# Optimization experiments

Measured on AMD Instinct MI355X. Metric: run time of the kernel, lower is better.

Reference implementation:

```python
import jax, jax.numpy as jnp
import numpy as np

T, B, D = 64, 256, 2000
TN, E, H, A, V = 3000, 256, 256, 128, 128
PS, PE, S = 64, 64, 128
G1N, G1L, G2N, G2L = 1500, 4, 1500, 6


def setup_inputs():
    key = jax.random.key(0)
    ks = jax.random.split(key, 32)
    def nrm(k, shape, s=0.05):
        return jax.random.normal(k, shape, dtype=jnp.float32) * s
    inp = {}
    inp["X"] = jax.random.uniform(ks[0], (T, B, D), dtype=jnp.float32)
    inp["profiles"] = nrm(ks[1], (B, PS), 1.0)
    inp["ini_embd"] = nrm(ks[2], (TN, E), 1.0)
    inp["Wa_w"] = nrm(ks[3], (2 * E, A))
    inp["Wa_b"] = jnp.zeros((A,), jnp.float32)
    inp["Ua_w"] = nrm(ks[4], (A, 1))
    inp["gru_Wih"] = nrm(ks[5], (3 * H, E))
    inp["gru_Whh"] = nrm(ks[6], (3 * H, H))
    inp["gru_bih"] = jnp.zeros((3 * H,), jnp.float32)
    inp["gru_bhh"] = jnp.zeros((3 * H,), jnp.float32)
    inp["tranH_w"] = nrm(ks[7], (H + PE, E))
    inp["tranH_b"] = jnp.zeros((E,), jnp.float32)
    inp["out_w"] = nrm(ks[8], (H + V + PE, D))
    inp["out_b"] = jnp.zeros((D,), jnp.float32)
    inp["erase_w"] = nrm(ks[9], (E, V))
    inp["erase_b"] = jnp.zeros((V,), jnp.float32)
    inp["add_w"] = nrm(ks[10], (E, V))
    inp["add_b"] = jnp.zeros((V,), jnp.float32)
    inp["iniVam"] = nrm(ks[11], (S, V), 1.0)
    inp["emP_w"] = nrm(ks[12], (PS, PE))
    inp["emP_b"] = jnp.zeros((PE,), jnp.float32)
    inp["attnP_w"] = nrm(ks[13], (PE + V, PE))
    inp["attnP_b"] = jnp.zeros((PE,), jnp.float32)
    inp["KMIds"] = jax.random.randint(ks[14], (S,), 0, TN, dtype=jnp.int32)
    inp["leaves1"] = jax.random.randint(ks[15], (G1N, G1L), 0, TN, dtype=jnp.int32)
    inp["anc1"] = jax.random.randint(ks[16], (G1N, G1L), 0, TN, dtype=jnp.int32)
    inp["leaves2"] = jax.random.randint(ks[17], (G2N, G2L), 0, TN, dtype=jnp.int32)
    inp["anc2"] = jax.random.randint(ks[18], (G2N, G2L), 0, TN, dtype=jnp.int32)
    inp["mapInfo"] = jax.random.randint(ks[19], (D,), 0, G1N + G2N, dtype=jnp.int32)
    lens = jnp.sort(jax.random.randint(ks[20], (B,), 1, T + 1, dtype=jnp.int32))[::-1]
    inp["X_lengths"] = lens.at[0].set(T)
    return inp


def _forward(floats, ints):
    (X, profiles, ini_embd, Wa_w, Wa_b, Ua_w, gru_Wih, gru_Whh, gru_bih, gru_bhh,
     tranH_w, tranH_b, out_w, out_b, erase_w, erase_b, add_w, add_b, iniVam,
     emP_w, emP_b, attnP_w, attnP_b) = floats
    KMIds, leaves1, anc1, leaves2, anc2, mapInfo, X_lengths = ints

    # GRAM-style ontology attention over (leaf, ancestor) pairs, grouped by path length
    def group_embed(leaves, anc):
        le = ini_embd[leaves]                                     # [N,L,E]
        ae = ini_embd[anc]                                        # [N,L,E]
        hdn = jnp.tanh(jnp.concatenate([le, ae], axis=2) @ Wa_w + Wa_b)
        w = jax.nn.softmax(hdn @ Ua_w, axis=1)                    # [N,L,1]
        return jnp.sum(w * ae, axis=1)                            # [N,E]

    embedMat = jnp.concatenate([group_embed(leaves1, anc1),
                                group_embed(leaves2, anc2)], axis=0)[mapInfo]  # [D,E]
    Xe = jnp.einsum('tbd,de->tbe', X, embedMat)                   # [T,B,E]

    # packed-sequence GRU: frozen state / zero output beyond each sample's length
    mask = (jnp.arange(T)[:, None] < X_lengths[None, :])[..., None]  # [T,B,1]

    def gru_step(h, tup):
        x_t, m_t = tup
        gx = x_t @ gru_Wih.T + gru_bih
        gh = h @ gru_Whh.T + gru_bhh
        r = jax.nn.sigmoid(gx[:, :H] + gh[:, :H])
        z = jax.nn.sigmoid(gx[:, H:2 * H] + gh[:, H:2 * H])
        n = jnp.tanh(gx[:, 2 * H:] + r * gh[:, 2 * H:])
        h_new = (1.0 - z) * n + z * h
        h = jnp.where(m_t, h_new, h)
        return h, jnp.where(m_t, h, 0.0)

    h0 = jnp.zeros((B, H), jnp.float32)
    _, gru_out = jax.lax.scan(gru_step, h0, (Xe, mask))           # [T,B,H]

    prof = profiles @ emP_w + emP_b                               # [B,PE]
    prof_rep = jnp.broadcast_to(prof[None], (T, B, PE))
    tran = jnp.concatenate([gru_out, prof_rep], axis=2) @ tranH_w + tranH_b  # [T,B,E]
    KM = ini_embd[KMIds]                                          # [S,E]
    slot_w = jax.nn.softmax(jnp.einsum('tbe,se->tbs', tran, KM), axis=2)     # [T,B,S]

    # erase/add gates depend only on Xe -> precompute, then scan VM recurrence
    erase = jax.nn.sigmoid(Xe @ erase_w + erase_b)                # [T,B,V]
    add = jnp.tanh(Xe @ add_w + add_b)                            # [T,B,V]

    def mem_step(VM, tup):
        sw, er, ad = tup                                          # [B,S],[B,V],[B,V]
        read = jnp.einsum('bs,bsv->bv', sw, VM)
        VM = VM * (1.0 - sw[:, :, None] * er[:, None, :]) + sw[:, :, None] * ad[:, None, :]
        return VM, read

    VM0 = jnp.broadcast_to(iniVam[None], (B, S, V))
    _, read = jax.lax.scan(mem_step, VM0, (slot_w, erase, add))   # read: [T,B,V]

    attn = jax.nn.relu(jnp.concatenate([prof_rep, read], axis=2) @ attnP_w + attnP_b)
    prof2 = prof_rep * attn
    final = jnp.concatenate([gru_out, read, prof2], axis=2)       # [T,B,H+V+PE]
    # dropout is identity (eval / drop_rate=0)
    return jax.nn.softmax(final @ out_w + out_b, axis=2)          # [T,B,D]


def reference(X, profiles, ini_embd, Wa_w, Wa_b, Ua_w, gru_Wih, gru_Whh, gru_bih, gru_bhh, tranH_w, tranH_b, out_w, out_b, erase_w, erase_b, add_w, add_b, iniVam, emP_w, emP_b, attnP_w, attnP_b, KMIds, leaves1, anc1, leaves2, anc2, mapInfo, X_lengths):
    floats = (X, profiles, ini_embd, Wa_w, Wa_b, Ua_w, gru_Wih, gru_Whh, gru_bih, gru_bhh,
              tranH_w, tranH_b, out_w, out_b, erase_w, erase_b, add_w, add_b, iniVam,
              emP_w, emP_b, attnP_w, attnP_b)
    ints = (KMIds, leaves1, anc1, leaves2, anc2, mapInfo, X_lengths)
    return _forward(floats, ints)
```

## Files before the change

### kernel.cpp

```cpp
#include <hip/hip_runtime.h>
#include <hip/hip_bf16.h>
#include <cmath>

#define T_  64
#define B_  256
#define D_  2000
#define TN_ 3000
#define E_  256
#define H_  256
#define A_  128
#define V_  128
#define PS_ 64
#define PE_ 64
#define S_  128
#define G1N_ 1500
#define G1L_ 4
#define G2N_ 1500
#define G2L_ 6
#define M_  (T_ * B_)
#define KF_ (H_ + V_ + PE_)

typedef __attribute__((ext_vector_type(8))) short short8_t;
typedef __attribute__((ext_vector_type(4))) float floatx4;
typedef _Float16 __attribute__((ext_vector_type(2))) h2_t;
typedef _Float16 __attribute__((ext_vector_type(8))) h8_t;

static __device__ __forceinline__ float sigmoidf_(float x) {
    return 1.0f / (1.0f + __expf(-x));
}

static __device__ __forceinline__ void bsplit_(float v, __hip_bfloat16& hi, __hip_bfloat16& lo) {
    hi = __float2bfloat16(v);
    lo = __float2bfloat16(v - __bfloat162float(hi));
}

static __device__ __forceinline__ float dot2_(unsigned int w, unsigned int h, float acc) {
    union { unsigned int u; h2_t h; } cw, ch;
    cw.u = w; ch.u = h;
#if __has_builtin(__builtin_amdgcn_fdot2)
    return __builtin_amdgcn_fdot2(cw.h, ch.h, acc, false);
#else
    return acc + (float)cw.h[0] * (float)ch.h[0] + (float)cw.h[1] * (float)ch.h[1];
#endif
}

static __device__ __forceinline__ void gl_lds16(const void* g, void* l)
{
#if __has_builtin(__builtin_amdgcn_global_load_lds)
    __builtin_amdgcn_global_load_lds(
        (const __attribute__((address_space(1))) void*)g,
        (__attribute__((address_space(3))) void*)l, 16, 0, 0);
#else
    *(short8_t*)l = *(const short8_t*)g;
#endif
}

template<int DT>
static __device__ __forceinline__ floatx4 mfma16_(short8_t a, short8_t b, floatx4 c) {
    if constexpr (DT == 0) {
        return __builtin_amdgcn_mfma_f32_16x16x32_bf16(a, b, c, 0, 0, 0);
    } else {
        union { short8_t s; h8_t h; } ua, ub;
        ua.s = a; ub.s = b;
        return __builtin_amdgcn_mfma_f32_16x16x32_f16(ua.h, ub.h, c, 0, 0, 0);
    }
}

template<int EPI, bool ACCUM, int OUTMODE, int NPH, int DT>
__global__ __launch_bounds__(256)
void k_mgemm3(const __hip_bfloat16* __restrict__ Ahi, const __hip_bfloat16* __restrict__ Alo,
              const __hip_bfloat16* __restrict__ Bhi, const __hip_bfloat16* __restrict__ Blo,
              const float* __restrict__ bias, float* __restrict__ Cf,
              __hip_bfloat16* __restrict__ Chi, __hip_bfloat16* __restrict__ Clo,
              int K, int Nreal, int nblk)
{
    __shared__ __align__(16) short As[2][4096];
    __shared__ __align__(16) short Bs[2][4096];

    const int tid  = threadIdx.x;
    const int lane = tid & 63;
    const int w    = tid >> 6;
    const int wm   = w >> 1, wn = w & 1;
    const int lr   = lane & 15;
    const int lkc  = lane >> 4;

    const int bx = blockIdx.x;
    const int xcd = bx & 7, loc = bx >> 3;
    const int mchunk = (int)gridDim.x / (8 * nblk);
    const int m0 = (xcd * mchunk + loc / nblk) * 128;
    const int n0 = (loc % nblk) * 128;

    const int fa = 2 * w;
    const size_t aoff0 = (size_t)(m0 + fa * 16 + lr) * K + lkc * 8;
    const size_t aoff1 = aoff0 + (size_t)16 * K;
    const size_t boff0 = (size_t)(n0 + fa * 16 + lr) * K + lkc * 8;
    const size_t boff1 = boff0 + (size_t)16 * K;

    const int lA0 = (fa    ) * 512 + lane * 8;
    const int lA1 = (fa + 1) * 512 + lane * 8;

    floatx4 acc[4][4];
#pragma unroll
    for (int i = 0; i < 4; ++i)
#pragma unroll
        for (int j = 0; j < 4; ++j) acc[i][j] = floatx4{0.f, 0.f, 0.f, 0.f};

    const int KT = K >> 5;
    const int NT = NPH * KT;

    int s_ph = 0, s_k = 0;
    auto do_stage = [&](int buf) {
        const __hip_bfloat16* Ap = (s_ph == 2) ? Alo : Ahi;
        const __hip_bfloat16* Bp = (s_ph == 1) ? Blo : Bhi;
        gl_lds16(Ap + aoff0 + s_k, &As[buf][lA0]);
        gl_lds16(Ap + aoff1 + s_k, &As[buf][lA1]);
        gl_lds16(Bp + boff0 + s_k, &Bs[buf][lA0]);
        gl_lds16(Bp + boff1 + s_k, &Bs[buf][lA1]);
        s_k += 32;
        if (s_k >= K) { s_k = 0; ++s_ph; }
    };

    do_stage(0);
    __syncthreads();

#pragma unroll 1
    for (int t = 0; t < NT; ++t) {
        const int cur = t & 1;
        if (t + 1 < NT) do_stage(cur ^ 1);

        short8_t af[4], bf[4];
#pragma unroll
        for (int i = 0; i < 4; ++i)
            af[i] = *(const short8_t*)(const void*)&As[cur][(wm * 4 + i) * 512 + lane * 8];
#pragma unroll
        for (int j = 0; j < 4; ++j)
            bf[j] = *(const short8_t*)(const void*)&Bs[cur][(wn * 4 + j) * 512 + lane * 8];
#pragma unroll
        for (int i = 0; i < 4; ++i)
#pragma unroll
            for (int j = 0; j < 4; ++j)
                acc[i][j] = mfma16_<DT>(af[i], bf[j], acc[i][j]);

        __syncthreads();
    }

#pragma unroll
    for (int i = 0; i < 4; ++i) {
        const int row = m0 + wm * 64 + i * 16 + (lane >> 4) * 4;
#pragma unroll
        for (int j = 0; j < 4; ++j) {
            const int col = n0 + wn * 64 + j * 16 + (lane & 15);
            if (col < Nreal) {
                float bv = bias ? bias[col] : 0.0f;
#pragma unroll
                for (int r = 0; r < 4; ++r) {
                    float v = acc[i][j][r] + bv;
                    if (EPI == 1) v = (col < 128) ? sigmoidf_(v) : tanhf(v);
                    if (EPI == 2) {
                        if (col < 128) v = sigmoidf_(v);
                        else if (col < 256) v = tanhf(v);
                    }
                    size_t o = (size_t)(row + r) * Nreal + col;
                    if (OUTMODE == 0) {
                        if (ACCUM) v += Cf[o];
                        Cf[o] = v;
                    } else if (OUTMODE == 1) {
                        __hip_bfloat16 h, l;
                        bsplit_(v, h, l);
                        Chi[o] = h; Clo[o] = l;
                    } else {
                        ((_Float16*)Chi)[o] = (_Float16)v;
                    }
                }
            }
        }
    }
}

__global__ __launch_bounds__(256)
void k_cvtX(const float* __restrict__ X, _Float16* __restrict__ XH)
{
    int idx = blockIdx.x * blockDim.x + threadIdx.x;
    if (idx >= M_ * 256) return;
    int m = idx >> 8, d0 = (idx & 255) * 8;
    _Float16 h[8];
    if (d0 + 7 < D_) {
        float4 p = *(const float4*)(X + (size_t)m * D_ + d0);
        float4 q = *(const float4*)(X + (size_t)m * D_ + d0 + 4);
        h[0]=(_Float16)p.x; h[1]=(_Float16)p.y; h[2]=(_Float16)p.z; h[3]=(_Float16)p.w;
        h[4]=(_Float16)q.x; h[5]=(_Float16)q.y; h[6]=(_Float16)q.z; h[7]=(_Float16)q.w;
    } else {
#pragma unroll
        for (int i = 0; i < 8; ++i)
            h[i] = (d0 + i < D_) ? (_Float16)X[(size_t)m * D_ + d0 + i] : (_Float16)0.0f;
    }
    *(short8_t*)(XH + (size_t)m * 2048 + d0) = *(short8_t*)h;
}

__global__ __launch_bounds__(256)
void k_mgemmXh(const _Float16* __restrict__ XH,
               const _Float16* __restrict__ Bhi, const _Float16* __restrict__ Blo,
               __hip_bfloat16* __restrict__ Chi, __hip_bfloat16* __restrict__ Clo)
{
    const int KP = 2048, NN = 256, nblk = 2;
    __shared__ __align__(16) short Ah[2][4096];
    __shared__ __align__(16) short Bh[2][4096];
    __shared__ __align__(16) short Bl[2][4096];

    const int tid  = threadIdx.x;
    const int lane = tid & 63;
    const int w    = tid >> 6;
    const int wm   = w >> 1, wn = w & 1;
    const int lr   = lane & 15;
    const int lkc  = lane >> 4;

    const int bx = blockIdx.x;
    const int xcd = bx & 7, loc = bx >> 3;
    const int mchunk = 256 / (8 * nblk);
    const int m0 = (xcd * mchunk + loc / nblk) * 128;
    const int n0 = (loc % nblk) * 128;

    const int fa = 2 * w;
    const size_t aoff0 = (size_t)(m0 + fa * 16 + lr) * KP + lkc * 8;
    const size_t aoff1 = aoff0 + (size_t)16 * KP;
    const size_t boff0 = (size_t)(n0 + fa * 16 + lr) * KP + lkc * 8;
    const size_t boff1 = boff0 + (size_t)16 * KP;

    const int lA0 = (fa    ) * 512 + lane * 8;
    const int lA1 = (fa + 1) * 512 + lane * 8;

    floatx4 acc[4][4];
#pragma unroll
    for (int i = 0; i < 4; ++i)
#pragma unroll
        for (int j = 0; j < 4; ++j) acc[i][j] = floatx4{0.f, 0.f, 0.f, 0.f};

    int s_k = 0;
    auto do_stage = [&](int buf) {
        gl_lds16(XH  + aoff0 + s_k, &Ah[buf][lA0]);
        gl_lds16(XH  + aoff1 + s_k, &Ah[buf][lA1]);
        gl_lds16(Bhi + boff0 + s_k, &Bh[buf][lA0]);
        gl_lds16(Bhi + boff1 + s_k, &Bh[buf][lA1]);
        gl_lds16(Blo + boff0 + s_k, &Bl[buf][lA0]);
        gl_lds16(Blo + boff1 + s_k, &Bl[buf][lA1]);
        s_k += 32;
    };

    do_stage(0);
    __syncthreads();

#pragma unroll 1
    for (int t = 0; t < KP / 32; ++t) {
        const int cur = t & 1;
        if (s_k < KP) do_stage(cur ^ 1);

        short8_t af[4], bfh[4], bfl[4];
#pragma unroll
        for (int i = 0; i < 4; ++i) {
            af[i]  = *(const short8_t*)(const void*)&Ah[cur][(wm * 4 + i) * 512 + lane * 8];
            bfh[i] = *(const short8_t*)(const void*)&Bh[cur][(wn * 4 + i) * 512 + lane * 8];
        }
#pragma unroll
        for (int i = 0; i < 4; ++i)
#pragma unroll
            for (int j = 0; j < 4; ++j)
                acc[i][j] = mfma16_<1>(af[i], bfh[j], acc[i][j]);
#pragma unroll
        for (int j = 0; j < 4; ++j)
            bfl[j] = *(const short8_t*)(const void*)&Bl[cur][(wn * 4 + j) * 512 + lane * 8];
#pragma unroll
        for (int i = 0; i < 4; ++i)
#pragma unroll
            for (int j = 0; j < 4; ++j)
                acc[i][j] = mfma16_<1>(af[i], bfl[j], acc[i][j]);

        __syncthreads();
    }

#pragma unroll
    for (int i = 0; i < 4; ++i) {
        const int row = m0 + wm * 64 + i * 16 + (lane >> 4) * 4;
#pragma unroll
        for (int j = 0; j < 4; ++j) {
            const int col = n0 + wn * 64 + j * 16 + (lane & 15);
#pragma unroll
            for (int r = 0; r < 4; ++r) {
                float v = acc[i][j][r];
                size_t o = (size_t)(row + r) * NN + col;
                __hip_bfloat16 h, l;
                bsplit_(v, h, l);
                Chi[o] = h; Clo[o] = l;
            }
        }
    }
}

template<int BM, int BN, int BK, int TM, int TN>
__global__ __launch_bounds__(256)
void k_gemm(const float* __restrict__ A, const float* __restrict__ B,
            float* __restrict__ C, int M, int N, int K)
{
    __shared__ float As[BK][BM + 4];
    __shared__ float Bs[BK][BN + 4];
    const int tid = threadIdx.y * blockDim.x + threadIdx.x;
    const int m0 = blockIdx.y * BM;
    const int n0 = blockIdx.x * BN;
    float acc[TM][TN];
#pragma unroll
    for (int i = 0; i < TM; ++i)
#pragma unroll
        for (int j = 0; j < TN; ++j) acc[i][j] = 0.0f;
    for (int k0 = 0; k0 < K; k0 += BK) {
#pragma unroll
        for (int i = tid; i < BM * BK; i += 256) {
            int r = i / BK, c = i % BK;
            int m = m0 + r;
            As[c][r] = (m < M) ? A[(size_t)m * K + k0 + c] : 0.0f;
        }
#pragma unroll
        for (int i = tid; i < BK * BN; i += 256) {
            int r = i / BN, c = i % BN;
            Bs[r][c] = B[(size_t)(k0 + r) * N + n0 + c];
        }
        __syncthreads();
#pragma unroll
        for (int kk = 0; kk < BK; ++kk) {
            float a[TM], b[TN];
#pragma unroll
            for (int i = 0; i < TM; ++i) a[i] = As[kk][threadIdx.y * TM + i];
#pragma unroll
            for (int j = 0; j < TN; ++j) b[j] = Bs[kk][threadIdx.x * TN + j];
#pragma unroll
            for (int i = 0; i < TM; ++i)
#pragma unroll
                for (int j = 0; j < TN; ++j) acc[i][j] += a[i] * b[j];
        }
        __syncthreads();
    }
#pragma unroll
    for (int i = 0; i < TM; ++i) {
        int m = m0 + threadIdx.y * TM + i;
        if (m >= M) continue;
#pragma unroll
        for (int j = 0; j < TN; ++j)
            C[(size_t)m * N + n0 + threadIdx.x * TN + j] = acc[i][j];
    }
}

__global__ __launch_bounds__(256)
void k_packall(const float* __restrict__ Wa_w,
               const float* __restrict__ erase_w, const float* __restrict__ add_w,
               const float* __restrict__ Wih,
               const float* __restrict__ erase_b, const float* __restrict__ add_b,
               const float* __restrict__ bih,
               const float* __restrict__ tranH_w, const float* __restrict__ out_w,
               const float* __restrict__ ini_embd, const int* __restrict__ KMIds,
               const float* __restrict__ Whh,
               float* __restrict__ W2p,
               __hip_bfloat16* __restrict__ WGhi, __hip_bfloat16* __restrict__ WGlo,
               float* __restrict__ biasG,
               __hip_bfloat16* __restrict__ THhi, __hip_bfloat16* __restrict__ THlo,
               _Float16* __restrict__ OWf,
               __hip_bfloat16* __restrict__ KMhi, __hip_bfloat16* __restrict__ KMlo,
               unsigned int* __restrict__ W4)
{
    int idx = blockIdx.x * blockDim.x + threadIdx.x;
    if (idx < 65536) {
        int e = idx >> 8, j = idx & 255;
        W2p[idx] = (j < A_) ? Wa_w[(size_t)e * A_ + j]
                            : Wa_w[(size_t)(E_ + e) * A_ + (j - A_)];
        return;
    }
    idx -= 65536;
    if (idx < 262144) {
        int n = idx >> 8, k = idx & 255;
        float v;
        if (n < 128)      v = erase_w[(size_t)k * V_ + n];
        else if (n < 256) v = add_w[(size_t)k * V_ + (n - 128)];
        else              v = Wih[(size_t)(n - 256) * 256 + k];
        bsplit_(v, WGhi[idx], WGlo[idx]);
        return;
    }
    idx -= 262144;
    if (idx < 1024) {
        biasG[idx] = (idx < 128) ? erase_b[idx]
                   : (idx < 256) ? add_b[idx - 128]
                                 : bih[idx - 256];
        return;
    }
    idx -= 1024;
    if (idx < 81920) {
        int n = idx / 320, k = idx % 320;
        bsplit_(tranH_w[(size_t)k * 256 + n], THhi[idx], THlo[idx]);
        return;
    }
    idx -= 81920;
    if (idx < 917504) {
        int n = idx / 448, k = idx % 448;
        OWf[idx] = (n < D_) ? (_Float16)out_w[(size_t)k * D_ + n] : (_Float16)0.0f;
        return;
    }
    idx -= 917504;
    if (idx < 32768) {
        int s = idx >> 8, k = idx & 255;
        bsplit_(ini_embd[(size_t)KMIds[s] * E_ + k], KMhi[idx], KMlo[idx]);
        return;
    }
    idx -= 32768;
    if (idx < 98304) {
        int j = idx / 128, e2 = idx % 128;
        union { unsigned int u; h2_t h; } c;
        c.h[0] = (_Float16)Whh[(size_t)j * 256 + 2 * e2];
        c.h[1] = (_Float16)Whh[(size_t)j * 256 + 2 * e2 + 1];
        int ch = e2 >> 2, i = e2 & 3;
        W4[((size_t)ch * 768 + j) * 4 + i] = c.u;
    }
}

__global__ void k_prof(const float* __restrict__ profiles, const float* __restrict__ emP_w,
                       const float* __restrict__ emP_b, float* __restrict__ prof)
{
    int b = blockIdx.x, j = threadIdx.x;
    float acc = emP_b[j];
    for (int k = 0; k < PS_; ++k) acc += profiles[(size_t)b * PS_ + k] * emP_w[(size_t)k * PE_ + j];
    prof[(size_t)b * PE_ + j] = acc;
}

__global__ void k_embMT_f16(const float* __restrict__ embG, const int* __restrict__ mapInfo,
                            _Float16* __restrict__ hi, _Float16* __restrict__ lo)
{
    int idx = blockIdx.x * blockDim.x + threadIdx.x;
    if (idx >= 256 * 2048) return;
    int e = idx >> 11, d = idx & 2047;
    float v = (d < D_) ? embG[(size_t)mapInfo[d] * E_ + e] : 0.0f;
    _Float16 h = (_Float16)v;
    hi[idx] = h;
    lo[idx] = (_Float16)(v - (float)h);
}

__global__ void k_group_embed(const float* __restrict__ PP, const float* __restrict__ Wa_b,
                              const float* __restrict__ Ua_w, const float* __restrict__ ini_embd,
                              const int* __restrict__ leaves1, const int* __restrict__ anc1,
                              const int* __restrict__ leaves2, const int* __restrict__ anc2,
                              float* __restrict__ embedG)
{
    int n = blockIdx.x;
    int lane = threadIdx.x;
    const int* lv; const int* ac; int L;
    if (n < G1N_) { L = G1L_; lv = leaves1 + (size_t)n * G1L_; ac = anc1 + (size_t)n * G1L_; }
    else { int n2 = n - G1N_; L = G2L_; lv = leaves2 + (size_t)n2 * G2L_; ac = anc2 + (size_t)n2 * G2L_; }

    float score[6]; int ai[6];
    for (int l = 0; l < L; ++l) {
        int li = lv[l]; int av = ac[l]; ai[l] = av;
        float s = 0.0f;
        for (int a = lane; a < A_; a += 64) {
            float hv = tanhf(PP[(size_t)li * 256 + a] + PP[(size_t)av * 256 + 128 + a] + Wa_b[a]);
            s += hv * Ua_w[a];
        }
        for (int o = 32; o; o >>= 1) s += __shfl_xor(s, o);
        score[l] = s;
    }
    float mx = -1e30f;
    for (int l = 0; l < L; ++l) mx = fmaxf(mx, score[l]);
    float w[6], sum = 0.0f;
    for (int l = 0; l < L; ++l) { w[l] = __expf(score[l] - mx); sum += w[l]; }
    float inv = 1.0f / sum;
    for (int e = lane; e < E_; e += 64) {
        float acc = 0.0f;
        for (int l = 0; l < L; ++l) acc += w[l] * inv * ini_embd[(size_t)ai[l] * E_ + e];
        embedG[(size_t)n * E_ + e] = acc;
    }
}

__global__ __launch_bounds__(768)
void k_gru7(const float* __restrict__ Cg, const uint4* __restrict__ W4,
            const float* __restrict__ bhh, const int* __restrict__ X_len,
            const float* __restrict__ prof, _Float16* __restrict__ F,
            __hip_bfloat16* __restrict__ At_hi, __hip_bfloat16* __restrict__ At_lo)
{
    const int b = blockIdx.x;
    const int tid = threadIdx.x;

    __shared__ uint4 h2S[32];
    __shared__ float ghS[768];
    __shared__ float gxnS[256];

    if (tid < 128) ((unsigned int*)h2S)[tid] = 0u;

    float hreg = 0.0f;
    const int len = X_len[b];
    const float bj = bhh[tid];

    __hip_bfloat16 phi, plo;
    if (tid >= 256 && tid < 320)
        bsplit_(prof[(size_t)b * PE_ + (tid - 256)], phi, plo);

    __syncthreads();

#define DOT8(BUF, BASE)                                                     \
    {                                                                       \
        _Pragma("unroll")                                                   \
        for (int s = 0; s < 8; ++s) {                                       \
            uint4 h = h2S[(BASE) + s];                                      \
            a0 = dot2_(BUF[s].x, h.x, a0);                                  \
            a0 = dot2_(BUF[s].y, h.y, a0);                                  \
            a0 = dot2_(BUF[s].z, h.z, a0);                                  \
            a0 = dot2_(BUF[s].w, h.w, a0);                                  \
        }                                                                   \
    }
#define LOAD8(BUF, BASE)                                                    \
    {                                                                       \
        _Pragma("unroll")                                                   \
        for (int s = 0; s < 8; ++s)                                         \
            BUF[s] = W4[(size_t)((BASE) + s) * 768 + tid];                  \
    }

    for (int t = 0; t < T_; ++t) {
        float gxv = Cg[((size_t)t * B_ + b) * 1024 + 256 + tid];

        uint4 wa[8], wb[8];
        LOAD8(wa, 0)
        float a0 = bj;
        LOAD8(wb, 8)
        DOT8(wa, 0)
        LOAD8(wa, 16)
        DOT8(wb, 8)
        LOAD8(wb, 24)
        DOT8(wa, 16)
        DOT8(wb, 24)

        if (tid < 512) ghS[tid] = a0 + gxv;
        else { ghS[tid] = a0; gxnS[tid - 512] = gxv; }
        __syncthreads();

        if (tid < 256) {
            float r  = sigmoidf_(ghS[tid]);
            float z  = sigmoidf_(ghS[256 + tid]);
            float nn = tanhf(gxnS[tid] + r * ghS[512 + tid]);
            float hnew = (1.0f - z) * nn + z * hreg;
            bool msk = (t < len);
            hreg = msk ? hnew : hreg;
            float ov = msk ? hreg : 0.0f;
            size_t m = (size_t)t * B_ + b;
            F[m * KF_ + tid] = (_Float16)ov;
            size_t o = m * 320 + tid;
            bsplit_(ov, At_hi[o], At_lo[o]);
            float partner = __shfl_xor(hreg, 1);
            if (!(tid & 1)) {
                union { unsigned int u; h2_t h; } p;
                p.h[0] = (_Float16)hreg;
                p.h[1] = (_Float16)partner;
                ((unsigned int*)h2S)[tid >> 1] = p.u;
            }
        } else if (tid < 320) {
            size_t o = ((size_t)t * B_ + b) * 320 + tid;
            At_hi[o] = phi;
            At_lo[o] = plo;
        }
        __syncthreads();
    }
#undef DOT8
#undef LOAD8
}

__global__ __launch_bounds__(256)
void k_memf(const float* __restrict__ slotw, const float* __restrict__ Cg,
            const float* __restrict__ iniVam, const float* __restrict__ prof,
            const float* __restrict__ attnP_w, const float* __restrict__ attnP_b,
            _Float16* __restrict__ F)
{
    const int b = blockIdx.x;
    const int tid = threadIdx.x;
    const int v = tid & (V_ - 1);
    const int sh = tid >> 7;
    const int sbase = sh * 64;

    __shared__ float aW[(PE_ + V_) * PE_];
    __shared__ float swL[S_];
    __shared__ float eaL[2 * V_];
    __shared__ float part[V_];
    __shared__ float rdL[V_];
    __shared__ float pfL[PE_];
    __shared__ float abL[PE_];
    __shared__ float pp[4][PE_];

    for (int i = tid; i < (PE_ + V_) * PE_; i += 256) aW[i] = attnP_w[i];
    if (tid < PE_) {
        pfL[tid] = prof[(size_t)b * PE_ + tid];
        abL[tid] = attnP_b[tid];
    }

    float VM[64];
#pragma unroll
    for (int i = 0; i < 64; ++i) VM[i] = iniVam[(size_t)(sbase + i) * V_ + v];
    __syncthreads();

    for (int t = 0; t < T_; ++t) {
        size_t m = (size_t)t * B_ + b;
        if (tid < S_) swL[tid] = slotw[m * S_ + tid];
        eaL[tid] = Cg[m * 1024 + tid];
        __syncthreads();

        if (tid < 64) {
            float a = swL[tid], bb = swL[64 + tid];
            float mx = fmaxf(a, bb);
            for (int o = 32; o; o >>= 1) mx = fmaxf(mx, __shfl_xor(mx, o));
            float e0 = __expf(a - mx), e1 = __expf(bb - mx);
            float s = e0 + e1;
            for (int o = 32; o; o >>= 1) s += __shfl_xor(s, o);
            float inv = 1.0f / s;
            swL[tid] = e0 * inv;
            swL[64 + tid] = e1 * inv;
        }
        __syncthreads();

        float er = eaL[v], ad = eaL[V_ + v];
        float p0 = 0.0f, p1 = 0.0f, p2 = 0.0f, p3 = 0.0f;
#pragma unroll
        for (int i = 0; i < 16; ++i) {
            float s0 = swL[sbase + 4 * i];
            float s1 = swL[sbase + 4 * i + 1];
            float s2 = swL[sbase + 4 * i + 2];
            float s3 = swL[sbase + 4 * i + 3];
            float v0 = VM[4 * i], v1 = VM[4 * i + 1], v2 = VM[4 * i + 2], v3 = VM[4 * i + 3];
            p0 += s0 * v0; p1 += s1 * v1; p2 += s2 * v2; p3 += s3 * v3;
            VM[4 * i]     = v0 * (1.0f - s0 * er) + s0 * ad;
            VM[4 * i + 1] = v1 * (1.0f - s1 * er) + s1 * ad;
            VM[4 * i + 2] = v2 * (1.0f - s2 * er) + s2 * ad;
            VM[4 * i + 3] = v3 * (1.0f - s3 * er) + s3 * ad;
        }
        float acc = (p0 + p1) + (p2 + p3);
        if (sh == 1) part[v] = acc;
        __syncthreads();
        if (sh == 0) {
            float rv = acc + part[v];
            rdL[v] = rv;
            F[m * KF_ + H_ + v] = (_Float16)rv;
        }
        __syncthreads();

        {
            const int pe = tid & 63, q = tid >> 6;
            float s = 0.0f;
            const int k0 = q * 48;
#pragma unroll
            for (int k = 0; k < 48; ++k) {
                int kk = k0 + k;
                float xv = (kk < PE_) ? pfL[kk] : rdL[kk - PE_];
                s += xv * aW[kk * PE_ + pe];
            }
            pp[q][pe] = s;
        }
        __syncthreads();
        if (tid < PE_) {
            float a = abL[tid] + ((pp[0][tid] + pp[1][tid]) + (pp[2][tid] + pp[3][tid]));
            a = fmaxf(a, 0.0f);
            F[m * KF_ + H_ + V_ + tid] = (_Float16)(pfL[tid] * a);
        }
        __syncthreads();
    }
}

__global__ __launch_bounds__(256)
void k_softmax2000(const _Float16* __restrict__ L, float* __restrict__ C)
{
    const int m = blockIdx.x;
    const size_t base = (size_t)m * D_;
    const int tid = threadIdx.x;
    const int wid = tid >> 6, lane = tid & 63;
    __shared__ float red[4], red2[4];

    float v[8];
#pragma unroll
    for (int i = 0; i < 8; ++i) {
        int d = i * 256 + tid;
        v[i] = (d < D_) ? (float)L[base + d] : -1e30f;
    }
    float mx = v[0];
#pragma unroll
    for (int i = 1; i < 8; ++i) mx = fmaxf(mx, v[i]);
    for (int o = 32; o; o >>= 1) mx = fmaxf(mx, __shfl_xor(mx, o));
    if (lane == 0) red[wid] = mx;
    __syncthreads();
    mx = fmaxf(fmaxf(red[0], red[1]), fmaxf(red[2], red[3]));

    float sum = 0.0f;
#pragma unroll
    for (int i = 0; i < 8; ++i) { v[i] = __expf(v[i] - mx); sum += v[i]; }
    for (int o = 32; o; o >>= 1) sum += __shfl_xor(sum, o);
    if (lane == 0) red2[wid] = sum;
    __syncthreads();
    sum = red2[0] + red2[1] + red2[2] + red2[3];
    float inv = 1.0f / sum;
#pragma unroll
    for (int i = 0; i < 8; ++i) {
        int d = i * 256 + tid;
        if (d < D_) C[base + d] = v[i] * inv;
    }
}

extern "C" void kernel_launch(void* const* d_in, const int* in_sizes, int n_in,
                              void* d_out, int out_size, void* d_ws, size_t ws_size,
                              hipStream_t stream)
{
    const float* X        = (const float*)d_in[0];
    const float* profiles = (const float*)d_in[1];
    const float* ini_embd = (const float*)d_in[2];
    const float* Wa_w     = (const float*)d_in[3];
    const float* Wa_b     = (const float*)d_in[4];
    const float* Ua_w     = (const float*)d_in[5];
    const float* gru_Wih  = (const float*)d_in[6];
    const float* gru_Whh  = (const float*)d_in[7];
    const float* gru_bih  = (const float*)d_in[8];
    const float* gru_bhh  = (const float*)d_in[9];
    const float* tranH_w  = (const float*)d_in[10];
    const float* tranH_b  = (const float*)d_in[11];
    const float* out_w    = (const float*)d_in[12];
    const float* out_b    = (const float*)d_in[13];
    const float* erase_w  = (const float*)d_in[14];
    const float* erase_b  = (const float*)d_in[15];
    const float* add_w    = (const float*)d_in[16];
    const float* add_b    = (const float*)d_in[17];
    const float* iniVam   = (const float*)d_in[18];
    const float* emP_w    = (const float*)d_in[19];
    const float* emP_b    = (const float*)d_in[20];
    const float* attnP_w  = (const float*)d_in[21];
    const float* attnP_b  = (const float*)d_in[22];
    const int* KMIds   = (const int*)d_in[23];
    const int* leaves1 = (const int*)d_in[24];
    const int* anc1    = (const int*)d_in[25];
    const int* leaves2 = (const int*)d_in[26];
    const int* anc2    = (const int*)d_in[27];
    const int* mapInfo = (const int*)d_in[28];
    const int* X_len   = (const int*)d_in[29];

    char* ws = (char*)d_ws;
    float* out = (float*)d_out;
    typedef __hip_bfloat16 bf16;

    const size_t R0 = 0;
    const size_t R1 = 67108864;
    const size_t R2 = 83886080;
    const size_t R3 = 100663296;
    size_t P = 121634816;
    const size_t EMBHI = P; P += 1048576;
    const size_t EMBLO = P; P += 1048576;
    const size_t OWF  = P; P += 1835008;
    const size_t WGHI = P; P += 524288;
    const size_t WGLO = P; P += 524288;
    const size_t THHI = P; P += 163840;
    const size_t THLO = P; P += 163840;
    const size_t KMHI = P; P += 65536;
    const size_t KMLO = P; P += 65536;
    const size_t W4O  = P; P += 393216;
    const size_t PROF = P; P += 65536;
    const size_t BIAS = P; P += 4096;
    const size_t W2O  = P; P += 262144;

    float* PP      = (float*)(ws + R0);
    float* embG    = (float*)(ws + R0 + 12288000);
    _Float16* XH   = (_Float16*)(ws + R0);
    float* Cg      = (float*)(ws + R0);
    _Float16* LG16 = (_Float16*)(ws + R0);
    _Float16* F16  = (_Float16*)(ws + R1);
    bf16*  Xe_hi   = (bf16*)(ws + R2);
    bf16*  Xe_lo   = (bf16*)(ws + R2 + 8388608);
    bf16*  tran_hi = (bf16*)(ws + R2);
    bf16*  tran_lo = (bf16*)(ws + R2 + 8388608);
    bf16*  At_hi   = (bf16*)(ws + R3);
    bf16*  At_lo   = (bf16*)(ws + R3 + 10485760);
    float* slotw   = (float*)(ws + R3);
    _Float16* EMBhi = (_Float16*)(ws + EMBHI);
    _Float16* EMBlo = (_Float16*)(ws + EMBLO);
    _Float16* OWf = (_Float16*)(ws + OWF);
    bf16*  WGhi = (bf16*)(ws + WGHI); bf16* WGlo = (bf16*)(ws + WGLO);
    bf16*  THhi = (bf16*)(ws + THHI); bf16* THlo = (bf16*)(ws + THLO);
    bf16*  KMhi = (bf16*)(ws + KMHI); bf16* KMlo = (bf16*)(ws + KMLO);
    unsigned int* W4 = (unsigned int*)(ws + W4O);
    float* prof  = (float*)(ws + PROF);
    float* biasG = (float*)(ws + BIAS);
    float* W2p   = (float*)(ws + W2O);

    k_packall<<<5700, 256, 0, stream>>>(Wa_w, erase_w, add_w, gru_Wih,
        erase_b, add_b, gru_bih, tranH_w, out_w, ini_embd, KMIds, gru_Whh,
        W2p, WGhi, WGlo, biasG, THhi, THlo, OWf, KMhi, KMlo, W4);
    k_prof<<<B_, PE_, 0, stream>>>(profiles, emP_w, emP_b, prof);

    {
        dim3 blk(16, 16);
        dim3 grid(4, (TN_ + 63) / 64);
        k_gemm<64, 64, 16, 4, 4><<<grid, blk, 0, stream>>>(ini_embd, W2p, PP, TN_, 256, E_);
    }
    k_group_embed<<<G1N_ + G2N_, 64, 0, stream>>>(PP, Wa_b, Ua_w, ini_embd,
                                                  leaves1, anc1, leaves2, anc2, embG);
    k_embMT_f16<<<(256 * 2048) / 256, 256, 0, stream>>>(embG, mapInfo, EMBhi, EMBlo);

    k_cvtX<<<(M_ * 256) / 256, 256, 0, stream>>>(X, XH);

    k_mgemmXh<<<128 * 2, 256, 0, stream>>>(XH, EMBhi, EMBlo, Xe_hi, Xe_lo);

    k_mgemm3<2, false, 0, 3, 0><<<128 * 8, 256, 0, stream>>>(Xe_hi, Xe_lo, WGhi, WGlo,
        biasG, Cg, nullptr, nullptr, 256, 1024, 8);

    k_gru7<<<256, 768, 0, stream>>>(Cg, (const uint4*)W4, gru_bhh, X_len, prof,
                                    F16, At_hi, At_lo);

    k_mgemm3<0, false, 1, 3, 0><<<128 * 2, 256, 0, stream>>>(At_hi, At_lo, THhi, THlo,
        tranH_b, nullptr, tran_hi, tran_lo, 320, 256, 2);

    k_mgemm3<0, false, 0, 3, 0><<<128 * 1, 256, 0, stream>>>(tran_hi, tran_lo, KMhi, KMlo,
        nullptr, slotw, nullptr, nullptr, 256, 128, 1);

    k_memf<<<B_, 256, 0, stream>>>(slotw, Cg, iniVam, prof, attnP_w, attnP_b, F16);

    k_mgemm3<0, false, 2, 1, 1><<<128 * 16, 256, 0, stream>>>(
        (const bf16*)F16, nullptr, (const bf16*)OWf, nullptr,
        out_b, nullptr, (bf16*)LG16, nullptr, 448, 2000, 16);

    k_softmax2000<<<M_, 256, 0, stream>>>(LG16, out);
}
```

Measured before the change: 693.7 us.

## Split memory-scan kernel: hoist slot softmax and attention out of sequential loop

The per-batch sequential memory kernel previously ran the slot-weight softmax and the profile-attention matvec inside its 64-step time loop. Both only depend on per-(t,b) data, so they now run in separate fully parallel kernels, one before and one after the scan. The scan kernel keeps only the read/update and writes the read vectors to a workspace buffer. This shortens the serial critical path and removes several barriers per step, at the cost of two extra launches and an extra global round trip of the read vectors.

```diff
diff --git a/kernel.cpp b/kernel.cpp
--- a/kernel.cpp
+++ b/kernel.cpp
@@ -564,11 +564,26 @@
 #undef LOAD8
 }
 
+__global__ void k_softmax128(float* __restrict__ C)
+{
+    const int m = blockIdx.x;
+    const size_t base = (size_t)m * S_;
+    const int lane = threadIdx.x;
+    float a = C[base + lane], b = C[base + 64 + lane];
+    float mx = fmaxf(a, b);
+    for (int o = 32; o; o >>= 1) mx = fmaxf(mx, __shfl_xor(mx, o));
+    float e0 = __expf(a - mx), e1 = __expf(b - mx);
+    float s = e0 + e1;
+    for (int o = 32; o; o >>= 1) s += __shfl_xor(s, o);
+    float inv = 1.0f / s;
+    C[base + lane] = e0 * inv;
+    C[base + 64 + lane] = e1 * inv;
+}
+
 __global__ __launch_bounds__(256)
-void k_memf(const float* __restrict__ slotw, const float* __restrict__ Cg,
-            const float* __restrict__ iniVam, const float* __restrict__ prof,
-            const float* __restrict__ attnP_w, const float* __restrict__ attnP_b,
-            _Float16* __restrict__ F)
+void k_mem(const float* __restrict__ slotw, const float* __restrict__ Cg,
+           const float* __restrict__ iniVam, float* __restrict__ readv,
+           _Float16* __restrict__ F)
 {
     const int b = blockIdx.x;
     const int tid = threadIdx.x;
@@ -576,43 +591,18 @@
     const int sh = tid >> 7;
     const int sbase = sh * 64;
 
-    __shared__ float aW[(PE_ + V_) * PE_];
+    float VM[64];
+#pragma unroll
+    for (int i = 0; i < 64; ++i) VM[i] = iniVam[(size_t)(sbase + i) * V_ + v];
+
     __shared__ float swL[S_];
     __shared__ float eaL[2 * V_];
     __shared__ float part[V_];
-    __shared__ float rdL[V_];
-    __shared__ float pfL[PE_];
-    __shared__ float abL[PE_];
-    __shared__ float pp[4][PE_];
-
-    for (int i = tid; i < (PE_ + V_) * PE_; i += 256) aW[i] = attnP_w[i];
-    if (tid < PE_) {
-        pfL[tid] = prof[(size_t)b * PE_ + tid];
-        abL[tid] = attnP_b[tid];
-    }
-
-    float VM[64];
-#pragma unroll
-    for (int i = 0; i < 64; ++i) VM[i] = iniVam[(size_t)(sbase + i) * V_ + v];
-    __syncthreads();
 
     for (int t = 0; t < T_; ++t) {
         size_t m = (size_t)t * B_ + b;
         if (tid < S_) swL[tid] = slotw[m * S_ + tid];
         eaL[tid] = Cg[m * 1024 + tid];
-        __syncthreads();
-
-        if (tid < 64) {
-            float a = swL[tid], bb = swL[64 + tid];
-            float mx = fmaxf(a, bb);
-            for (int o = 32; o; o >>= 1) mx = fmaxf(mx, __shfl_xor(mx, o));
-            float e0 = __expf(a - mx), e1 = __expf(bb - mx);
-            float s = e0 + e1;
-            for (int o = 32; o; o >>= 1) s += __shfl_xor(s, o);
-            float inv = 1.0f / s;
-            swL[tid] = e0 * inv;
-            swL[64 + tid] = e1 * inv;
-        }
         __syncthreads();
 
         float er = eaL[v], ad = eaL[V_ + v];
@@ -635,31 +625,33 @@
         __syncthreads();
         if (sh == 0) {
             float rv = acc + part[v];
-            rdL[v] = rv;
+            readv[m * V_ + v] = rv;
             F[m * KF_ + H_ + v] = (_Float16)rv;
         }
         __syncthreads();
-
-        {
-            const int pe = tid & 63, q = tid >> 6;
-            float s = 0.0f;
-            const int k0 = q * 48;
-#pragma unroll
-            for (int k = 0; k < 48; ++k) {
-                int kk = k0 + k;
-                float xv = (kk < PE_) ? pfL[kk] : rdL[kk - PE_];
-                s += xv * aW[kk * PE_ + pe];
-            }
-            pp[q][pe] = s;
-        }
-        __syncthreads();
-        if (tid < PE_) {
-            float a = abL[tid] + ((pp[0][tid] + pp[1][tid]) + (pp[2][tid] + pp[3][tid]));
-            a = fmaxf(a, 0.0f);
-            F[m * KF_ + H_ + V_ + tid] = (_Float16)(pfL[tid] * a);
-        }
-        __syncthreads();
-    }
+    }
+}
+
+__global__ __launch_bounds__(64)
+void k_attn(const float* __restrict__ readv, const float* __restrict__ prof,
+            const float* __restrict__ attnP_w, const float* __restrict__ attnP_b,
+            _Float16* __restrict__ F)
+{
+    const int m = blockIdx.x;
+    const int b = m & (B_ - 1);
+    const int pe = threadIdx.x;
+    __shared__ float rd[V_];
+    __shared__ float pf[PE_];
+    rd[pe] = readv[(size_t)m * V_ + pe];
+    rd[64 + pe] = readv[(size_t)m * V_ + 64 + pe];
+    pf[pe] = prof[(size_t)b * PE_ + pe];
+    __syncthreads();
+
+    float a = attnP_b[pe];
+    for (int k = 0; k < PE_; ++k) a += pf[k] * attnP_w[(size_t)k * PE_ + pe];
+    for (int k = 0; k < V_; ++k) a += rd[k] * attnP_w[(size_t)(PE_ + k) * PE_ + pe];
+    a = fmaxf(a, 0.0f);
+    F[(size_t)m * KF_ + H_ + V_ + pe] = (_Float16)(pf[pe] * a);
 }
 
 __global__ __launch_bounds__(256)
@@ -771,6 +763,7 @@
     bf16*  At_hi   = (bf16*)(ws + R3);
     bf16*  At_lo   = (bf16*)(ws + R3 + 10485760);
     float* slotw   = (float*)(ws + R3);
+    float* readv   = (float*)(ws + R3 + 10485760);
     _Float16* EMBhi = (_Float16*)(ws + EMBHI);
     _Float16* EMBlo = (_Float16*)(ws + EMBLO);
     _Float16* OWf = (_Float16*)(ws + OWF);
@@ -812,7 +805,9 @@
     k_mgemm3<0, false, 0, 3, 0><<<128 * 1, 256, 0, stream>>>(tran_hi, tran_lo, KMhi, KMlo,
         nullptr, slotw, nullptr, nullptr, 256, 128, 1);
 
-    k_memf<<<B_, 256, 0, stream>>>(slotw, Cg, iniVam, prof, attnP_w, attnP_b, F16);
+    k_softmax128<<<M_, 64, 0, stream>>>(slotw);
+    k_mem<<<B_, 256, 0, stream>>>(slotw, Cg, iniVam, readv, F16);
+    k_attn<<<M_, 64, 0, stream>>>(readv, prof, attnP_w, attnP_b, F16);
 
     k_mgemm3<0, false, 2, 1, 1><<<128 * 16, 256, 0, stream>>>(
         (const bf16*)F16, nullptr, (const bf16*)OWf, nullptr,
```

Result: faster. 657.1 us (-5.3%).
